# Performance work log

Measured on AMD Instinct MI355X. Metric: run time of the kernel, lower is better.

Reference implementation:

```python
import jax, jax.numpy as jnp
import numpy as np

N_NODES = 50000
N_EDGES = 600000
D_IN = 128
D_OUT = 128


def setup_inputs() -> dict:
    key = jax.random.key(0)
    k1, k2, k3, k4 = jax.random.split(key, 4)
    mpg_ft = jax.random.normal(k1, (N_NODES, D_IN), dtype=jnp.float32)
    edge_index = jax.random.randint(k2, (2, N_EDGES), 0, N_NODES, dtype=jnp.int64)
    # GCNConv linear params (PyG: glorot weight [in, out], zero bias)
    limit = (6.0 / (D_IN + D_OUT)) ** 0.5
    W = jax.random.uniform(k3, (D_IN, D_OUT), dtype=jnp.float32, minval=-limit, maxval=limit)
    b = jnp.zeros((D_OUT,), dtype=jnp.float32)
    return {"mpg_ft": mpg_ft, "edge_index": edge_index, "W": W, "b": b}


def gcn_conv(x, edge_index, W, b):
    n = x.shape[0]
    # add self-loops (PyG GCNConv default)
    loops = jnp.arange(n, dtype=edge_index.dtype)
    src = jnp.concatenate([edge_index[0], loops])
    dst = jnp.concatenate([edge_index[1], loops])
    # symmetric normalization: deg computed on destination with unit edge weights
    deg = jax.ops.segment_sum(jnp.ones_like(dst, dtype=x.dtype), dst, num_segments=n)
    dis = jnp.where(deg > 0, jax.lax.rsqrt(jnp.maximum(deg, 1.0)), 0.0)
    norm = dis[src] * dis[dst]                      # [E+N]
    h = x @ W                                        # [N, D_OUT]
    msg = h[src] * norm[:, None]                     # [E+N, D_OUT] gather
    out = jax.ops.segment_sum(msg, dst, num_segments=n)  # scatter-add
    return out + b


def reference(mpg_ft, edge_index, W, b):
    # freeze=True: x = g.mpg_ft; conv=True: x = GCNConv(x, edge_index)
    return gcn_conv(mpg_ft, edge_index, W, b)
```

## Files before the change

kernel.cpp:

```cpp
#include <hip/hip_runtime.h>

#define D 128
#define CAP 64
#define NBLK_A 128
#define SUBCAP 64
#define BINSHIFT 8

typedef __bf16 bf16x8 __attribute__((ext_vector_type(8)));
typedef float f32x4 __attribute__((ext_vector_type(4)));

static __device__ __forceinline__ unsigned short f2bf(float x) {
    unsigned int u = __builtin_bit_cast(unsigned int, x);
    unsigned int r = u + 0x7fffu + ((u >> 16) & 1u);
    return (unsigned short)(r >> 16);
}
static __device__ __forceinline__ float bitf(unsigned int u) {
    return __builtin_bit_cast(float, u);
}

__global__ __launch_bounds__(256) void k1_kernel(const int* __restrict__ ei,
                                                 const float* __restrict__ W,
                                                 unsigned int* __restrict__ counts,
                                                 unsigned int* __restrict__ binned,
                                                 unsigned short* __restrict__ wt, int E) {
    int t = threadIdx.x;
    int k = blockIdx.x;
    if (k < NBLK_A) {
        __shared__ unsigned int hist[256];
        hist[t] = 0u;
        __syncthreads();
        int chunk = (E + NBLK_A - 1) / NBLK_A;
        int s0 = k * chunk, s1 = min(E, s0 + chunk);
        const int* dstp = ei + E;
        for (int e = s0 + t; e < s1; e += 256) atomicAdd(&hist[dstp[e] >> BINSHIFT], 1u);
        __syncthreads();
        counts[k * 256 + t] = hist[t];
        __syncthreads();
        hist[t] = 0u;
        __syncthreads();
        for (int e = s0 + t; e < s1; e += 256) {
            int src = ei[e];
            int d = dstp[e];
            int bin = d >> BINSHIFT;
            unsigned int off = atomicAdd(&hist[bin], 1u);
            binned[((unsigned)bin * NBLK_A + (unsigned)k) * SUBCAP + off] =
                ((unsigned)d << 16) | (unsigned)src;
        }
    } else {
        int tid = (k - NBLK_A) * 256 + t;
        for (int i = tid; i < D * D; i += 8 * 256) {
            int r = i >> 7, c = i & 127;
            wt[c * 128 + r] = f2bf(W[i]);
        }
    }
}

__global__ __launch_bounds__(256) void k2_kernel(const unsigned int* __restrict__ counts,
                                                 const unsigned int* __restrict__ binned,
                                                 const float* __restrict__ x,
                                                 const unsigned short* __restrict__ wt,
                                                 unsigned int* __restrict__ cnt,
                                                 float* __restrict__ disf,
                                                 unsigned short* __restrict__ bucket,
                                                 unsigned short* __restrict__ hs, int n, int NB) {
    __shared__ char smem[48 * 1024];
    int t = threadIdx.x;
    int bid = blockIdx.x;

    if (bid < NB) {
        unsigned int* lcnt = (unsigned int*)smem;
        lcnt[t] = 0u;
        __syncthreads();
        int wv = t >> 6, ln = t & 63;
        int b = bid;
        for (int k = wv; k < NBLK_A; k += 4) {
            int m = (int)counts[k * 256 + b];
            unsigned int base = ((unsigned)b * NBLK_A + (unsigned)k) * SUBCAP;
            for (int i = ln; i < m; i += 64) {
                unsigned int p = binned[base + i];
                unsigned int d = p >> 16;
                unsigned int src = p & 0xffffu;
                unsigned int slot = atomicAdd(&lcnt[d & 255u], 1u);
                bucket[(size_t)d * CAP + (slot & (CAP - 1))] = (unsigned short)src;
            }
        }
        __syncthreads();
        int node = (b << BINSHIFT) + t;
        if (node < n) {
            unsigned int c = lcnt[t];
            cnt[node] = c;
            disf[node] = rsqrtf((float)c + 1.0f);
        }
        return;
    }

    uint4* Xs = (uint4*)smem;
    uint4* Ws = (uint4*)smem + 1024;
    int rowbase = (bid - NB) * 64;

    const uint4* wg = (const uint4*)wt;
#pragma unroll
    for (int j = 0; j < 8; ++j) {
        int gi = t + j * 256;
        int r = gi >> 4, s = gi & 15;
        Ws[r * 16 + (s ^ (r & 7))] = wg[gi];
    }
    const float4* x4 = (const float4*)x;
#pragma unroll
    for (int j = 0; j < 4; ++j) {
        int gi = t + j * 256;
        int r = gi >> 4, s = gi & 15;
        uint4 v = make_uint4(0u, 0u, 0u, 0u);
        int grow = rowbase + r;
        if (grow < n) {
            float4 f0 = x4[(size_t)grow * 32 + s * 2];
            float4 f1 = x4[(size_t)grow * 32 + s * 2 + 1];
            v.x = f2bf(f0.x) | ((unsigned)f2bf(f0.y) << 16);
            v.y = f2bf(f0.z) | ((unsigned)f2bf(f0.w) << 16);
            v.z = f2bf(f1.x) | ((unsigned)f2bf(f1.y) << 16);
            v.w = f2bf(f1.z) | ((unsigned)f2bf(f1.w) << 16);
        }
        Xs[r * 16 + (s ^ (r & 7))] = v;
    }
    __syncthreads();

    int w = t >> 6, l = t & 63;
    int lr = l & 15, lg = l >> 4;
    f32x4 acc[4][2] = {};

#pragma unroll
    for (int kt = 0; kt < 4; ++kt) {
        int ks = kt * 4 + lg;
        bf16x8 bfr[2];
#pragma unroll
        for (int ct = 0; ct < 2; ++ct) {
            int nc = w * 32 + ct * 16 + lr;
            bfr[ct] = __builtin_bit_cast(bf16x8, Ws[nc * 16 + (ks ^ (nc & 7))]);
        }
#pragma unroll
        for (int mt = 0; mt < 4; ++mt) {
            int mr = mt * 16 + lr;
            bf16x8 afr = __builtin_bit_cast(bf16x8, Xs[mr * 16 + (ks ^ (mr & 7))]);
            acc[mt][0] = __builtin_amdgcn_mfma_f32_16x16x32_bf16(afr, bfr[0], acc[mt][0], 0, 0, 0);
            acc[mt][1] = __builtin_amdgcn_mfma_f32_16x16x32_bf16(afr, bfr[1], acc[mt][1], 0, 0, 0);
        }
    }

#pragma unroll
    for (int mt = 0; mt < 4; ++mt) {
        int row0 = rowbase + mt * 16 + lg * 4;
#pragma unroll
        for (int r = 0; r < 4; ++r) {
            int grow = row0 + r;
            if (grow < n) {
#pragma unroll
                for (int ct = 0; ct < 2; ++ct) {
                    int col = w * 32 + ct * 16 + lr;
                    hs[(size_t)grow * 128 + col] = f2bf(acc[mt][ct][r]);
                }
            }
        }
    }
}

#define ACC8F(A0, A1, U, DS)                       \
    do {                                           \
        A0.x += bitf((U).x << 16) * DS;            \
        A0.y += bitf((U).x & 0xffff0000u) * DS;    \
        A0.z += bitf((U).y << 16) * DS;            \
        A0.w += bitf((U).y & 0xffff0000u) * DS;    \
        A1.x += bitf((U).z << 16) * DS;            \
        A1.y += bitf((U).z & 0xffff0000u) * DS;    \
        A1.z += bitf((U).w << 16) * DS;            \
        A1.w += bitf((U).w & 0xffff0000u) * DS;    \
    } while (0)

__global__ __launch_bounds__(256) void gather_kernel(const unsigned short* __restrict__ bucket,
                                                     const unsigned int* __restrict__ cnt,
                                                     const float* __restrict__ disf,
                                                     const unsigned short* __restrict__ hs,
                                                     const float* __restrict__ b,
                                                     float* __restrict__ out, int n) {
    int node = (blockIdx.x * 256 + threadIdx.x) >> 4;
    int l = threadIdx.x & 15;
    if (node >= n) return;
    unsigned int c = cnt[node];
    float dn = disf[node];
    const unsigned short* seg = bucket + (size_t)node * CAP;
    const uint4* h4 = (const uint4*)hs;

    uint4 u = h4[(size_t)node * 16 + l];
    float4 aA0 = make_float4(bitf(u.x << 16) * dn, bitf(u.x & 0xffff0000u) * dn,
                             bitf(u.y << 16) * dn, bitf(u.y & 0xffff0000u) * dn);
    float4 aA1 = make_float4(bitf(u.z << 16) * dn, bitf(u.z & 0xffff0000u) * dn,
                             bitf(u.w << 16) * dn, bitf(u.w & 0xffff0000u) * dn);
    float4 aB0 = make_float4(0.f, 0.f, 0.f, 0.f);
    float4 aB1 = make_float4(0.f, 0.f, 0.f, 0.f);

    for (unsigned int base = 0; base < c; base += 16) {
        int m = min(16u, c - base);
        int v = 0;
        float dv = 0.f;
        if (l < m) {
            v = (int)seg[base + l];
            dv = disf[v];
        }
        int j = 0;
        for (; j + 3 < m; j += 4) {
            int s0 = __shfl(v, j, 16);
            int s1 = __shfl(v, j + 1, 16);
            int s2 = __shfl(v, j + 2, 16);
            int s3 = __shfl(v, j + 3, 16);
            float d0 = __shfl(dv, j, 16);
            float d1 = __shfl(dv, j + 1, 16);
            float d2 = __shfl(dv, j + 2, 16);
            float d3 = __shfl(dv, j + 3, 16);
            uint4 u0 = h4[(size_t)s0 * 16 + l];
            uint4 u1 = h4[(size_t)s1 * 16 + l];
            uint4 u2 = h4[(size_t)s2 * 16 + l];
            uint4 u3 = h4[(size_t)s3 * 16 + l];
            ACC8F(aA0, aA1, u0, d0);
            ACC8F(aB0, aB1, u1, d1);
            ACC8F(aA0, aA1, u2, d2);
            ACC8F(aB0, aB1, u3, d3);
        }
        for (; j < m; ++j) {
            int s0 = __shfl(v, j, 16);
            float d0 = __shfl(dv, j, 16);
            uint4 u0 = h4[(size_t)s0 * 16 + l];
            ACC8F(aA0, aA1, u0, d0);
        }
    }

    float4 bv0 = ((const float4*)b)[l * 2];
    float4 bv1 = ((const float4*)b)[l * 2 + 1];
    float4 r0 = make_float4((aA0.x + aB0.x) * dn + bv0.x, (aA0.y + aB0.y) * dn + bv0.y,
                            (aA0.z + aB0.z) * dn + bv0.z, (aA0.w + aB0.w) * dn + bv0.w);
    float4 r1 = make_float4((aA1.x + aB1.x) * dn + bv1.x, (aA1.y + aB1.y) * dn + bv1.y,
                            (aA1.z + aB1.z) * dn + bv1.z, (aA1.w + aB1.w) * dn + bv1.w);
    float4* o4 = (float4*)out;
    o4[(size_t)node * 32 + l * 2] = r0;
    o4[(size_t)node * 32 + l * 2 + 1] = r1;
}

extern "C" void kernel_launch(void* const* d_in, const int* in_sizes, int n_in,
                              void* d_out, int out_size, void* d_ws, size_t ws_size,
                              hipStream_t stream) {
    const float* x = (const float*)d_in[0];
    const int* ei = (const int*)d_in[1];
    const float* W = (const float*)d_in[2];
    const float* b = (const float*)d_in[3];
    float* out = (float*)d_out;

    int n = in_sizes[0] / D;
    int E = in_sizes[1] / 2;
    int NB = (n + 255) >> 8;

    unsigned int* counts = (unsigned int*)d_ws;
    unsigned int* cnt = counts + NBLK_A * 256;
    float* disf = (float*)(cnt + n);
    unsigned int* binned = (unsigned int*)(disf + n);
    unsigned short* bucket = (unsigned short*)(binned + (size_t)NB * NBLK_A * SUBCAP);
    unsigned short* hs = bucket + (size_t)n * CAP;
    unsigned short* wt = hs + (size_t)n * D;

    k1_kernel<<<NBLK_A + 8, 256, 0, stream>>>(ei, W, counts, binned, wt, E);
    k2_kernel<<<NB + (n + 63) / 64, 256, 0, stream>>>(counts, binned, x, wt, cnt, disf, bucket,
                                                      hs, n, NB);
    gather_kernel<<<(n * 16 + 255) / 256, 256, 0, stream>>>(bucket, cnt, disf, hs, b, out, n);
}
```

Measured before the change: 70.39 us.

## Fuse bucketing and gather into one persistent kernel with grid barriers

Moves the dense transform (with on-the-fly W transpose to bf16) into the edge-binning kernel. Bucket construction now happens in shared memory inside a new 1024-thread gather kernel, with software grid barriers between the degree phase and four column-slice gather passes. This removes one launch and the global bucket array round-trip. In exchange it relies on all NB blocks being co-resident for the spin barriers, and it adds barrier latency plus fewer threads per node.

```diff
diff --git a/kernel.cpp b/kernel.cpp
--- a/kernel.cpp
+++ b/kernel.cpp
@@ -4,6 +4,7 @@
 #define CAP 64
 #define NBLK_A 128
 #define SUBCAP 64
+#define BSTR 66
 #define BINSHIFT 8
 
 typedef __bf16 bf16x8 __attribute__((ext_vector_type(8)));
@@ -18,23 +19,41 @@
     return __builtin_bit_cast(float, u);
 }
 
+static __device__ __forceinline__ void gbar(unsigned int* ctr, unsigned int target) {
+    __syncthreads();
+    if (threadIdx.x == 0) {
+        __threadfence();
+        __hip_atomic_fetch_add(ctr, 1u, __ATOMIC_ACQ_REL, __HIP_MEMORY_SCOPE_AGENT);
+        while (__hip_atomic_load(ctr, __ATOMIC_ACQUIRE, __HIP_MEMORY_SCOPE_AGENT) < target) {
+            __builtin_amdgcn_s_sleep(16);
+        }
+        __threadfence();
+    }
+    __syncthreads();
+}
+
 __global__ __launch_bounds__(256) void k1_kernel(const int* __restrict__ ei,
                                                  const float* __restrict__ W,
+                                                 const float* __restrict__ x,
                                                  unsigned int* __restrict__ counts,
                                                  unsigned int* __restrict__ binned,
-                                                 unsigned short* __restrict__ wt, int E) {
+                                                 unsigned int* __restrict__ ctrs,
+                                                 unsigned short* __restrict__ hs, int n, int E) {
+    __shared__ char smem[48 * 1024];
     int t = threadIdx.x;
-    int k = blockIdx.x;
-    if (k < NBLK_A) {
-        __shared__ unsigned int hist[256];
+    int bid = blockIdx.x;
+    if (bid == 0 && t < 8) ctrs[t] = 0u;
+
+    if (bid < NBLK_A) {
+        unsigned int* hist = (unsigned int*)smem;
         hist[t] = 0u;
         __syncthreads();
         int chunk = (E + NBLK_A - 1) / NBLK_A;
-        int s0 = k * chunk, s1 = min(E, s0 + chunk);
+        int s0 = bid * chunk, s1 = min(E, s0 + chunk);
         const int* dstp = ei + E;
         for (int e = s0 + t; e < s1; e += 256) atomicAdd(&hist[dstp[e] >> BINSHIFT], 1u);
         __syncthreads();
-        counts[k * 256 + t] = hist[t];
+        counts[bid * 256 + t] = hist[t];
         __syncthreads();
         hist[t] = 0u;
         __syncthreads();
@@ -43,67 +62,24 @@
             int d = dstp[e];
             int bin = d >> BINSHIFT;
             unsigned int off = atomicAdd(&hist[bin], 1u);
-            binned[((unsigned)bin * NBLK_A + (unsigned)k) * SUBCAP + off] =
+            binned[((unsigned)bin * NBLK_A + (unsigned)bid) * SUBCAP + off] =
                 ((unsigned)d << 16) | (unsigned)src;
-        }
-    } else {
-        int tid = (k - NBLK_A) * 256 + t;
-        for (int i = tid; i < D * D; i += 8 * 256) {
-            int r = i >> 7, c = i & 127;
-            wt[c * 128 + r] = f2bf(W[i]);
-        }
-    }
-}
-
-__global__ __launch_bounds__(256) void k2_kernel(const unsigned int* __restrict__ counts,
-                                                 const unsigned int* __restrict__ binned,
-                                                 const float* __restrict__ x,
-                                                 const unsigned short* __restrict__ wt,
-                                                 unsigned int* __restrict__ cnt,
-                                                 float* __restrict__ disf,
-                                                 unsigned short* __restrict__ bucket,
-                                                 unsigned short* __restrict__ hs, int n, int NB) {
-    __shared__ char smem[48 * 1024];
-    int t = threadIdx.x;
-    int bid = blockIdx.x;
-
-    if (bid < NB) {
-        unsigned int* lcnt = (unsigned int*)smem;
-        lcnt[t] = 0u;
-        __syncthreads();
-        int wv = t >> 6, ln = t & 63;
-        int b = bid;
-        for (int k = wv; k < NBLK_A; k += 4) {
-            int m = (int)counts[k * 256 + b];
-            unsigned int base = ((unsigned)b * NBLK_A + (unsigned)k) * SUBCAP;
-            for (int i = ln; i < m; i += 64) {
-                unsigned int p = binned[base + i];
-                unsigned int d = p >> 16;
-                unsigned int src = p & 0xffffu;
-                unsigned int slot = atomicAdd(&lcnt[d & 255u], 1u);
-                bucket[(size_t)d * CAP + (slot & (CAP - 1))] = (unsigned short)src;
-            }
-        }
-        __syncthreads();
-        int node = (b << BINSHIFT) + t;
-        if (node < n) {
-            unsigned int c = lcnt[t];
-            cnt[node] = c;
-            disf[node] = rsqrtf((float)c + 1.0f);
         }
         return;
     }
 
     uint4* Xs = (uint4*)smem;
     uint4* Ws = (uint4*)smem + 1024;
-    int rowbase = (bid - NB) * 64;
-
-    const uint4* wg = (const uint4*)wt;
-#pragma unroll
-    for (int j = 0; j < 8; ++j) {
-        int gi = t + j * 256;
-        int r = gi >> 4, s = gi & 15;
-        Ws[r * 16 + (s ^ (r & 7))] = wg[gi];
+    int rowbase = (bid - NBLK_A) * 64;
+
+    for (int cell = t; cell < 2048; cell += 256) {
+        int nc = cell >> 4, s = cell & 15;
+        const float* col = W + (s * 8) * 128 + nc;
+        unsigned int a0 = f2bf(col[0]) | ((unsigned)f2bf(col[128]) << 16);
+        unsigned int a1 = f2bf(col[256]) | ((unsigned)f2bf(col[384]) << 16);
+        unsigned int a2 = f2bf(col[512]) | ((unsigned)f2bf(col[640]) << 16);
+        unsigned int a3 = f2bf(col[768]) | ((unsigned)f2bf(col[896]) << 16);
+        Ws[nc * 16 + (s ^ (nc & 7))] = make_uint4(a0, a1, a2, a3);
     }
     const float4* x4 = (const float4*)x;
 #pragma unroll
@@ -163,84 +139,86 @@
     }
 }
 
-#define ACC8F(A0, A1, U, DS)                       \
-    do {                                           \
-        A0.x += bitf((U).x << 16) * DS;            \
-        A0.y += bitf((U).x & 0xffff0000u) * DS;    \
-        A0.z += bitf((U).y << 16) * DS;            \
-        A0.w += bitf((U).y & 0xffff0000u) * DS;    \
-        A1.x += bitf((U).z << 16) * DS;            \
-        A1.y += bitf((U).z & 0xffff0000u) * DS;    \
-        A1.z += bitf((U).w << 16) * DS;            \
-        A1.w += bitf((U).w & 0xffff0000u) * DS;    \
+#define ACC8F(A0, A1, U, DS)                    \
+    do {                                        \
+        A0.x += bitf((U).x << 16) * DS;         \
+        A0.y += bitf((U).x & 0xffff0000u) * DS; \
+        A0.z += bitf((U).y << 16) * DS;         \
+        A0.w += bitf((U).y & 0xffff0000u) * DS; \
+        A1.x += bitf((U).z << 16) * DS;         \
+        A1.y += bitf((U).z & 0xffff0000u) * DS; \
+        A1.z += bitf((U).w << 16) * DS;         \
+        A1.w += bitf((U).w & 0xffff0000u) * DS; \
     } while (0)
 
-__global__ __launch_bounds__(256) void gather_kernel(const unsigned short* __restrict__ bucket,
-                                                     const unsigned int* __restrict__ cnt,
-                                                     const float* __restrict__ disf,
-                                                     const unsigned short* __restrict__ hs,
-                                                     const float* __restrict__ b,
-                                                     float* __restrict__ out, int n) {
-    int node = (blockIdx.x * 256 + threadIdx.x) >> 4;
-    int l = threadIdx.x & 15;
-    if (node >= n) return;
-    unsigned int c = cnt[node];
-    float dn = disf[node];
-    const unsigned short* seg = bucket + (size_t)node * CAP;
-    const uint4* h4 = (const uint4*)hs;
-
-    uint4 u = h4[(size_t)node * 16 + l];
-    float4 aA0 = make_float4(bitf(u.x << 16) * dn, bitf(u.x & 0xffff0000u) * dn,
-                             bitf(u.y << 16) * dn, bitf(u.y & 0xffff0000u) * dn);
-    float4 aA1 = make_float4(bitf(u.z << 16) * dn, bitf(u.z & 0xffff0000u) * dn,
-                             bitf(u.w << 16) * dn, bitf(u.w & 0xffff0000u) * dn);
-    float4 aB0 = make_float4(0.f, 0.f, 0.f, 0.f);
-    float4 aB1 = make_float4(0.f, 0.f, 0.f, 0.f);
-
-    for (unsigned int base = 0; base < c; base += 16) {
-        int m = min(16u, c - base);
-        int v = 0;
-        float dv = 0.f;
-        if (l < m) {
-            v = (int)seg[base + l];
-            dv = disf[v];
-        }
-        int j = 0;
-        for (; j + 3 < m; j += 4) {
-            int s0 = __shfl(v, j, 16);
-            int s1 = __shfl(v, j + 1, 16);
-            int s2 = __shfl(v, j + 2, 16);
-            int s3 = __shfl(v, j + 3, 16);
-            float d0 = __shfl(dv, j, 16);
-            float d1 = __shfl(dv, j + 1, 16);
-            float d2 = __shfl(dv, j + 2, 16);
-            float d3 = __shfl(dv, j + 3, 16);
-            uint4 u0 = h4[(size_t)s0 * 16 + l];
-            uint4 u1 = h4[(size_t)s1 * 16 + l];
-            uint4 u2 = h4[(size_t)s2 * 16 + l];
-            uint4 u3 = h4[(size_t)s3 * 16 + l];
-            ACC8F(aA0, aA1, u0, d0);
-            ACC8F(aB0, aB1, u1, d1);
-            ACC8F(aA0, aA1, u2, d2);
-            ACC8F(aB0, aB1, u3, d3);
-        }
-        for (; j < m; ++j) {
-            int s0 = __shfl(v, j, 16);
-            float d0 = __shfl(dv, j, 16);
-            uint4 u0 = h4[(size_t)s0 * 16 + l];
-            ACC8F(aA0, aA1, u0, d0);
-        }
-    }
-
-    float4 bv0 = ((const float4*)b)[l * 2];
-    float4 bv1 = ((const float4*)b)[l * 2 + 1];
-    float4 r0 = make_float4((aA0.x + aB0.x) * dn + bv0.x, (aA0.y + aB0.y) * dn + bv0.y,
-                            (aA0.z + aB0.z) * dn + bv0.z, (aA0.w + aB0.w) * dn + bv0.w);
-    float4 r1 = make_float4((aA1.x + aB1.x) * dn + bv1.x, (aA1.y + aB1.y) * dn + bv1.y,
-                            (aA1.z + aB1.z) * dn + bv1.z, (aA1.w + aB1.w) * dn + bv1.w);
-    float4* o4 = (float4*)out;
-    o4[(size_t)node * 32 + l * 2] = r0;
-    o4[(size_t)node * 32 + l * 2 + 1] = r1;
+__global__ __launch_bounds__(1024) void k3_kernel(const unsigned int* __restrict__ counts,
+                                                  const unsigned int* __restrict__ binned,
+                                                  float* __restrict__ disf,
+                                                  const unsigned short* __restrict__ hs,
+                                                  const float* __restrict__ bias,
+                                                  unsigned int* __restrict__ ctrs,
+                                                  float* __restrict__ out, int n, int NB) {
+    __shared__ unsigned short sbucket[256 * BSTR];
+    __shared__ unsigned int lcnt[256];
+    int t = threadIdx.x;
+    int b = blockIdx.x;
+
+    if (t < 256) lcnt[t] = 0u;
+    __syncthreads();
+
+    int wv = t >> 6, ln = t & 63;
+    for (int k = wv; k < NBLK_A; k += 16) {
+        int m = (int)counts[k * 256 + b];
+        unsigned int base = ((unsigned)b * NBLK_A + (unsigned)k) * SUBCAP;
+        for (int i = ln; i < m; i += 64) {
+            unsigned int p = binned[base + i];
+            unsigned int d = p >> 16;
+            unsigned int src = p & 0xffffu;
+            unsigned int slot = atomicAdd(&lcnt[d & 255u], 1u);
+            sbucket[(d & 255u) * BSTR + (slot & (CAP - 1))] = (unsigned short)src;
+        }
+    }
+    __syncthreads();
+
+    if (t < 256) {
+        int nd = (b << BINSHIFT) + t;
+        if (nd < n) disf[nd] = rsqrtf((float)lcnt[t] + 1.0f);
+    }
+    gbar(&ctrs[0], (unsigned)NB);
+
+    int local = t >> 2, l = t & 3;
+    int node = (b << BINSHIFT) + local;
+    bool valid = node < n;
+    unsigned int c = valid ? lcnt[local] : 0u;
+    float dn = rsqrtf((float)c + 1.0f);
+    const unsigned short* sb = &sbucket[local * BSTR];
+
+    for (int p = 0; p < 4; ++p) {
+        if (valid) {
+            int coff = p * 32 + l * 8;
+            uint4 u = *(const uint4*)(hs + ((size_t)node << 7) + coff);
+            float4 a0 = make_float4(bitf(u.x << 16) * dn, bitf(u.x & 0xffff0000u) * dn,
+                                    bitf(u.y << 16) * dn, bitf(u.y & 0xffff0000u) * dn);
+            float4 a1 = make_float4(bitf(u.z << 16) * dn, bitf(u.z & 0xffff0000u) * dn,
+                                    bitf(u.w << 16) * dn, bitf(u.w & 0xffff0000u) * dn);
+#pragma unroll 4
+            for (int j = 0; j < (int)c; ++j) {
+                int s = (int)sb[j];
+                float ds = disf[s];
+                uint4 uu = *(const uint4*)(hs + ((size_t)s << 7) + coff);
+                ACC8F(a0, a1, uu, ds);
+            }
+            float4 bv0 = *(const float4*)(bias + coff);
+            float4 bv1 = *(const float4*)(bias + coff + 4);
+            float4 r0 = make_float4(a0.x * dn + bv0.x, a0.y * dn + bv0.y, a0.z * dn + bv0.z,
+                                    a0.w * dn + bv0.w);
+            float4 r1 = make_float4(a1.x * dn + bv1.x, a1.y * dn + bv1.y, a1.z * dn + bv1.z,
+                                    a1.w * dn + bv1.w);
+            *(float4*)(out + ((size_t)node << 7) + coff) = r0;
+            *(float4*)(out + ((size_t)node << 7) + coff + 4) = r1;
+        }
+        if (p < 3) gbar(&ctrs[1 + p], (unsigned)NB);
+    }
 }
 
 extern "C" void kernel_launch(void* const* d_in, const int* in_sizes, int n_in,
@@ -257,15 +235,12 @@
     int NB = (n + 255) >> 8;
 
     unsigned int* counts = (unsigned int*)d_ws;
-    unsigned int* cnt = counts + NBLK_A * 256;
-    float* disf = (float*)(cnt + n);
+    unsigned int* ctrs = counts + NBLK_A * 256;
+    float* disf = (float*)(ctrs + 8);
     unsigned int* binned = (unsigned int*)(disf + n);
-    unsigned short* bucket = (unsigned short*)(binned + (size_t)NB * NBLK_A * SUBCAP);
-    unsigned short* hs = bucket + (size_t)n * CAP;
-    unsigned short* wt = hs + (size_t)n * D;
-
-    k1_kernel<<<NBLK_A + 8, 256, 0, stream>>>(ei, W, counts, binned, wt, E);
-    k2_kernel<<<NB + (n + 63) / 64, 256, 0, stream>>>(counts, binned, x, wt, cnt, disf, bucket,
-                                                      hs, n, NB);
-    gather_kernel<<<(n * 16 + 255) / 256, 256, 0, stream>>>(bucket, cnt, disf, hs, b, out, n);
-}
+    unsigned short* hs = (unsigned short*)(binned + (size_t)NB * NBLK_A * SUBCAP);
+
+    k1_kernel<<<NBLK_A + (n + 63) / 64, 256, 0, stream>>>(ei, W, x, counts, binned, ctrs, hs, n,
+                                                          E);
+    k3_kernel<<<NB, 1024, 0, stream>>>(counts, binned, disf, hs, b, ctrs, out, n, NB);
+}
```

Result: slower. 201.0 us (+185.6%).

## Move GEMM into binning kernel and convert W to bf16 inline per block

Applied to the files above, without the earlier changes.

The x@W GEMM blocks now run in the first kernel alongside the edge-binning blocks, and the bucket-fill pass becomes a small standalone second kernel. Each GEMM block now transposes and converts W from fp32 to bf16 straight into shared memory, so the separate wt staging buffer is gone. This overlaps the compute-bound GEMM with the memory-bound binning and shortens the second kernel. The cost is that every GEMM block does strided fp32 reads of all of W, and the first kernel now reserves 48KB of shared memory even for its binning blocks.

```diff
diff --git a/kernel.cpp b/kernel.cpp
--- a/kernel.cpp
+++ b/kernel.cpp
@@ -20,21 +20,24 @@
 
 __global__ __launch_bounds__(256) void k1_kernel(const int* __restrict__ ei,
                                                  const float* __restrict__ W,
+                                                 const float* __restrict__ x,
                                                  unsigned int* __restrict__ counts,
                                                  unsigned int* __restrict__ binned,
-                                                 unsigned short* __restrict__ wt, int E) {
+                                                 unsigned short* __restrict__ hs, int n, int E) {
+    __shared__ char smem[48 * 1024];
     int t = threadIdx.x;
-    int k = blockIdx.x;
-    if (k < NBLK_A) {
-        __shared__ unsigned int hist[256];
+    int bid = blockIdx.x;
+
+    if (bid < NBLK_A) {
+        unsigned int* hist = (unsigned int*)smem;
         hist[t] = 0u;
         __syncthreads();
         int chunk = (E + NBLK_A - 1) / NBLK_A;
-        int s0 = k * chunk, s1 = min(E, s0 + chunk);
+        int s0 = bid * chunk, s1 = min(E, s0 + chunk);
         const int* dstp = ei + E;
         for (int e = s0 + t; e < s1; e += 256) atomicAdd(&hist[dstp[e] >> BINSHIFT], 1u);
         __syncthreads();
-        counts[k * 256 + t] = hist[t];
+        counts[bid * 256 + t] = hist[t];
         __syncthreads();
         hist[t] = 0u;
         __syncthreads();
@@ -43,67 +46,24 @@
             int d = dstp[e];
             int bin = d >> BINSHIFT;
             unsigned int off = atomicAdd(&hist[bin], 1u);
-            binned[((unsigned)bin * NBLK_A + (unsigned)k) * SUBCAP + off] =
+            binned[((unsigned)bin * NBLK_A + (unsigned)bid) * SUBCAP + off] =
                 ((unsigned)d << 16) | (unsigned)src;
-        }
-    } else {
-        int tid = (k - NBLK_A) * 256 + t;
-        for (int i = tid; i < D * D; i += 8 * 256) {
-            int r = i >> 7, c = i & 127;
-            wt[c * 128 + r] = f2bf(W[i]);
-        }
-    }
-}
-
-__global__ __launch_bounds__(256) void k2_kernel(const unsigned int* __restrict__ counts,
-                                                 const unsigned int* __restrict__ binned,
-                                                 const float* __restrict__ x,
-                                                 const unsigned short* __restrict__ wt,
-                                                 unsigned int* __restrict__ cnt,
-                                                 float* __restrict__ disf,
-                                                 unsigned short* __restrict__ bucket,
-                                                 unsigned short* __restrict__ hs, int n, int NB) {
-    __shared__ char smem[48 * 1024];
-    int t = threadIdx.x;
-    int bid = blockIdx.x;
-
-    if (bid < NB) {
-        unsigned int* lcnt = (unsigned int*)smem;
-        lcnt[t] = 0u;
-        __syncthreads();
-        int wv = t >> 6, ln = t & 63;
-        int b = bid;
-        for (int k = wv; k < NBLK_A; k += 4) {
-            int m = (int)counts[k * 256 + b];
-            unsigned int base = ((unsigned)b * NBLK_A + (unsigned)k) * SUBCAP;
-            for (int i = ln; i < m; i += 64) {
-                unsigned int p = binned[base + i];
-                unsigned int d = p >> 16;
-                unsigned int src = p & 0xffffu;
-                unsigned int slot = atomicAdd(&lcnt[d & 255u], 1u);
-                bucket[(size_t)d * CAP + (slot & (CAP - 1))] = (unsigned short)src;
-            }
-        }
-        __syncthreads();
-        int node = (b << BINSHIFT) + t;
-        if (node < n) {
-            unsigned int c = lcnt[t];
-            cnt[node] = c;
-            disf[node] = rsqrtf((float)c + 1.0f);
         }
         return;
     }
 
     uint4* Xs = (uint4*)smem;
     uint4* Ws = (uint4*)smem + 1024;
-    int rowbase = (bid - NB) * 64;
-
-    const uint4* wg = (const uint4*)wt;
-#pragma unroll
-    for (int j = 0; j < 8; ++j) {
-        int gi = t + j * 256;
-        int r = gi >> 4, s = gi & 15;
-        Ws[r * 16 + (s ^ (r & 7))] = wg[gi];
+    int rowbase = (bid - NBLK_A) * 64;
+
+    for (int cell = t; cell < 2048; cell += 256) {
+        int nc = cell >> 4, s = cell & 15;
+        const float* col = W + (s * 8) * 128 + nc;
+        unsigned int a0 = f2bf(col[0]) | ((unsigned)f2bf(col[128]) << 16);
+        unsigned int a1 = f2bf(col[256]) | ((unsigned)f2bf(col[384]) << 16);
+        unsigned int a2 = f2bf(col[512]) | ((unsigned)f2bf(col[640]) << 16);
+        unsigned int a3 = f2bf(col[768]) | ((unsigned)f2bf(col[896]) << 16);
+        Ws[nc * 16 + (s ^ (nc & 7))] = make_uint4(a0, a1, a2, a3);
     }
     const float4* x4 = (const float4*)x;
 #pragma unroll
@@ -163,16 +123,47 @@
     }
 }
 
-#define ACC8F(A0, A1, U, DS)                       \
-    do {                                           \
-        A0.x += bitf((U).x << 16) * DS;            \
-        A0.y += bitf((U).x & 0xffff0000u) * DS;    \
-        A0.z += bitf((U).y << 16) * DS;            \
-        A0.w += bitf((U).y & 0xffff0000u) * DS;    \
-        A1.x += bitf((U).z << 16) * DS;            \
-        A1.y += bitf((U).z & 0xffff0000u) * DS;    \
-        A1.z += bitf((U).w << 16) * DS;            \
-        A1.w += bitf((U).w & 0xffff0000u) * DS;    \
+__global__ __launch_bounds__(256) void k2_kernel(const unsigned int* __restrict__ counts,
+                                                 const unsigned int* __restrict__ binned,
+                                                 unsigned int* __restrict__ cnt,
+                                                 float* __restrict__ disf,
+                                                 unsigned short* __restrict__ bucket, int n) {
+    __shared__ unsigned int lcnt[256];
+    int t = threadIdx.x;
+    int b = blockIdx.x;
+    lcnt[t] = 0u;
+    __syncthreads();
+    int wv = t >> 6, ln = t & 63;
+    for (int k = wv; k < NBLK_A; k += 4) {
+        int m = (int)counts[k * 256 + b];
+        unsigned int base = ((unsigned)b * NBLK_A + (unsigned)k) * SUBCAP;
+        for (int i = ln; i < m; i += 64) {
+            unsigned int p = binned[base + i];
+            unsigned int d = p >> 16;
+            unsigned int src = p & 0xffffu;
+            unsigned int slot = atomicAdd(&lcnt[d & 255u], 1u);
+            bucket[(size_t)d * CAP + (slot & (CAP - 1))] = (unsigned short)src;
+        }
+    }
+    __syncthreads();
+    int node = (b << BINSHIFT) + t;
+    if (node < n) {
+        unsigned int c = lcnt[t];
+        cnt[node] = c;
+        disf[node] = rsqrtf((float)c + 1.0f);
+    }
+}
+
+#define ACC8F(A0, A1, U, DS)                    \
+    do {                                        \
+        A0.x += bitf((U).x << 16) * DS;         \
+        A0.y += bitf((U).x & 0xffff0000u) * DS; \
+        A0.z += bitf((U).y << 16) * DS;         \
+        A0.w += bitf((U).y & 0xffff0000u) * DS; \
+        A1.x += bitf((U).z << 16) * DS;         \
+        A1.y += bitf((U).z & 0xffff0000u) * DS; \
+        A1.z += bitf((U).w << 16) * DS;         \
+        A1.w += bitf((U).w & 0xffff0000u) * DS; \
     } while (0)
 
 __global__ __launch_bounds__(256) void gather_kernel(const unsigned short* __restrict__ bucket,
@@ -262,10 +253,8 @@
     unsigned int* binned = (unsigned int*)(disf + n);
     unsigned short* bucket = (unsigned short*)(binned + (size_t)NB * NBLK_A * SUBCAP);
     unsigned short* hs = bucket + (size_t)n * CAP;
-    unsigned short* wt = hs + (size_t)n * D;
-
-    k1_kernel<<<NBLK_A + 8, 256, 0, stream>>>(ei, W, counts, binned, wt, E);
-    k2_kernel<<<NB + (n + 63) / 64, 256, 0, stream>>>(counts, binned, x, wt, cnt, disf, bucket,
-                                                      hs, n, NB);
+
+    k1_kernel<<<NBLK_A + (n + 63) / 64, 256, 0, stream>>>(ei, W, x, counts, binned, hs, n, E);
+    k2_kernel<<<NB, 256, 0, stream>>>(counts, binned, cnt, disf, bucket, n);
     gather_kernel<<<(n * 16 + 255) / 256, 256, 0, stream>>>(bucket, cnt, disf, hs, b, out, n);
 }
```

New measurement: 94.30 us. +34.0%, slower.
